# Kernel tuning notes

Measured on AMD Instinct MI355X. Metric: run time of the kernel, lower is better.

Reference implementation:

```python
import jax, jax.numpy as jnp
import numpy as np

# Problem sizes (see shape_source)
C = 4096                      # sparse matrix is C x C
NUMEL = C * C                 # 16,777,216
S = 3355443                   # round(NUMEL * 0.2) sampled gradient entries
R = 1048576                   # result_quantity (top-k buffer size)
DECAY = 0.95                  # decay_constant
FRAC = S / float(NUMEL)       # fractional_sparsity (mask_active=False branch)


def setup_inputs() -> dict:
    key = jax.random.key(0)
    k1, k2, k3, k4 = jax.random.split(key, 4)
    # Sampled linear indices into the C x C grid (forward: torch.randint(0, numel, [S]))
    sample_index = jax.random.randint(k1, (S,), 0, NUMEL, dtype=jnp.int32)
    # Steady-state buffer of (row, col) pairs and their running gradient magnitudes
    result_index = jax.random.randint(k2, (R, 2), 0, C, dtype=jnp.int32)
    result_value = jax.random.uniform(k3, (R,), dtype=jnp.float32)
    # Incoming gradient on the sampled accumulator entries
    gradient = jax.random.normal(k4, (S,), dtype=jnp.float32)
    return {
        "sample_index": sample_index,
        "result_index": result_index,
        "result_value": result_value,
        "gradient": gradient,
    }


def reference(sample_index, result_index, result_value, gradient):
    """Faithful JAX version of StochasticSubSampler's backward-hook update:
    decay the stored buffer, take |gradient| on the new samples, coalesce
    duplicated (row, col) entries by summation, then keep the top-R values.
    Returns (new_result_index [R,2] int32, new_result_value [R] float32)."""
    adj_decay = 1.0 - FRAC * (1.0 - DECAY)  # adjusted decay constant

    # Linearized keys for coalescing. sample_index is already row*C + col.
    samp_keys = sample_index
    res_keys = result_index[:, 0] * C + result_index[:, 1]
    keys = jnp.concatenate([samp_keys, res_keys])               # [K]
    vals = jnp.concatenate([jnp.abs(gradient), adj_decay * result_value])  # [K]
    K = keys.shape[0]

    # Coalesce: sum values that share the same (row, col) key.
    uniq, inv = jnp.unique(keys, size=K, fill_value=-1, return_inverse=True)
    summed = jax.ops.segment_sum(vals, inv, num_segments=K)     # [K]
    counts = jax.ops.segment_sum(jnp.ones_like(vals), inv, num_segments=K)
    neg = jnp.finfo(jnp.float32).min
    summed = jnp.where(counts > 0, summed, neg)  # mask padded unique slots

    # Descending sort + top-R selection (argsort(-v)[:R] in the original).
    top_vals, top_pos = jax.lax.top_k(summed, R)
    top_keys = uniq[top_pos]
    new_index = jnp.stack([top_keys // C, top_keys % C], axis=-1)  # [R, 2]
    return new_index, top_vals
```

## Files before the change

kernel.cpp:

```cpp
#include <hip/hip_runtime.h>
#include <stdint.h>

#define CDIM   4096
#define S_N    3355443
#define R_N    1048576
#define N1     (S_N + R_N)
#define TILE   4096
#define NTILES ((N1 + TILE - 1) / TILE)
#define NPAD   (NTILES * TILE)
#define NSB    (NPAD / 256)
#define PAD_KEY 0xFFFFFFu
#define PAD_VAL 0xFFFFFFFFu

static __device__ __forceinline__ unsigned blockScanExcl(unsigned v, unsigned t,
                                                         unsigned* lw, unsigned* tot){
  unsigned lane = t & 63u, w = t >> 6;
  unsigned x = v;
  #pragma unroll
  for (int off = 1; off < 64; off <<= 1){
    unsigned y = __shfl_up(x, off, 64);
    if (lane >= (unsigned)off) x += y;
  }
  if (lane == 63u) lw[w] = x;
  __syncthreads();
  unsigned woff = 0;
  for (unsigned i = 0; i < w; i++) woff += lw[i];
  *tot = lw[0] + lw[1] + lw[2] + lw[3];
  __syncthreads();
  return x + woff - v;
}

__global__ __launch_bounds__(256) void k_build(const int* __restrict__ sidx,
                                               const int* __restrict__ ridx,
                                               const float* __restrict__ rval,
                                               const float* __restrict__ grad,
                                               uint64_t* __restrict__ A){
  unsigned i = blockIdx.x * 256u + threadIdx.x;
  uint32_t key, vb;
  if (i < S_N){
    key = (uint32_t)sidx[i];
    vb  = __float_as_uint(fabsf(grad[i]));
  } else if (i < N1){
    unsigned j = i - S_N;
    key = (uint32_t)(ridx[2u*j] * CDIM + ridx[2u*j + 1u]);
    const float ADJF = (float)(1.0 - (3355443.0 / 16777216.0) * (1.0 - 0.95));
    vb = __float_as_uint(ADJF * rval[j]);
  } else {
    key = PAD_KEY; vb = PAD_VAL;
  }
  A[i] = ((uint64_t)key << 32) | (uint64_t)vb;
}

__global__ __launch_bounds__(256) void k_hist(const uint64_t* __restrict__ in, unsigned shift,
                                              unsigned* __restrict__ gh){
  __shared__ unsigned h[256];
  unsigned t = threadIdx.x;
  h[t] = 0; __syncthreads();
  size_t base = (size_t)blockIdx.x * TILE;
  #pragma unroll
  for (int r = 0; r < 16; r++){
    uint64_t e = in[base + (size_t)r*256 + t];
    atomicAdd(&h[(unsigned)((e >> shift) & 0xFF)], 1u);
  }
  __syncthreads();
  gh[t * NTILES + blockIdx.x] = h[t];
}

__global__ __launch_bounds__(256) void k_scanrows(unsigned* __restrict__ gh,
                                                  unsigned* __restrict__ dtot){
  __shared__ unsigned lw[4];
  unsigned d = blockIdx.x, t = threadIdx.x;
  unsigned carry = 0;
  for (unsigned base = 0; base < NTILES; base += 256){
    unsigned i = base + t;
    unsigned v = (i < NTILES) ? gh[d * NTILES + i] : 0u;
    unsigned tot;
    unsigned e = blockScanExcl(v, t, lw, &tot);
    if (i < NTILES) gh[d * NTILES + i] = e + carry;
    carry += tot;
  }
  if (t == 0) dtot[d] = carry;
}

template <bool FINAL>
__device__ __forceinline__ void scatter_body(const uint64_t* __restrict__ in,
                                             uint64_t* __restrict__ out,
                                             float* __restrict__ fout,
                                             unsigned shift,
                                             const unsigned* __restrict__ gh,
                                             const unsigned* __restrict__ dtot){
  __shared__ unsigned wrun[4*256];
  __shared__ unsigned gput[256];
  __shared__ unsigned lw[4];
  __shared__ uint64_t stage[TILE];
  unsigned t = threadIdx.x, lane = t & 63u, w = t >> 6;
  wrun[t] = 0; wrun[256+t] = 0; wrun[512+t] = 0; wrun[768+t] = 0;
  __syncthreads();
  uint64_t ltm = (lane == 0) ? 0ull : (~0ull >> (64u - lane));
  uint64_t elems[16]; unsigned rnk[16]; unsigned dg[16];
  size_t base = (size_t)blockIdx.x * TILE + (size_t)w * 1024;
  #pragma unroll
  for (int r = 0; r < 16; r++){
    uint64_t e = in[base + (size_t)r*64 + lane];
    elems[r] = e;
    unsigned d = (unsigned)((e >> shift) & 0xFF);
    uint64_t m = ~0ull;
    #pragma unroll
    for (int b = 0; b < 8; b++){
      uint64_t bb = __ballot((d >> b) & 1u);
      m &= ((d >> b) & 1u) ? bb : ~bb;
    }
    unsigned rr   = (unsigned)__popcll(m & ltm);
    unsigned prev = wrun[w*256 + d];
    __builtin_amdgcn_wave_barrier();
    if (rr == 0) wrun[w*256 + d] = prev + (unsigned)__popcll(m);
    __builtin_amdgcn_wave_barrier();
    rnk[r] = prev + rr;
    dg[r]  = d;
  }
  __syncthreads();
  {
    unsigned d = t;
    unsigned c0 = wrun[d], c1 = wrun[256+d], c2 = wrun[512+d], c3 = wrun[768+d];
    unsigned cnt = c0 + c1 + c2 + c3;
    unsigned tot;
    unsigned ldig  = blockScanExcl(cnt, t, lw, &tot);
    unsigned tot2;
    unsigned dbase = blockScanExcl(dtot[d], t, lw, &tot2);
    gput[d] = dbase + gh[d * NTILES + blockIdx.x] - ldig;
    wrun[d]       = ldig;
    wrun[256 + d] = ldig + c0;
    wrun[512 + d] = ldig + c0 + c1;
    wrun[768 + d] = ldig + c0 + c1 + c2;
  }
  __syncthreads();
  #pragma unroll
  for (int r = 0; r < 16; r++)
    stage[ wrun[w*256 + dg[r]] + rnk[r] ] = elems[r];
  __syncthreads();
  #pragma unroll
  for (int r = 0; r < 16; r++){
    unsigned j = (unsigned)r * 256u + t;
    uint64_t e = stage[j];
    unsigned d = (unsigned)((e >> shift) & 0xFF);
    unsigned dest = gput[d] + j;
    if (FINAL){
      if (dest < R_N){
        uint32_t key = (uint32_t)(e >> 32);
        fout[2u*dest]        = (float)(key >> 12);
        fout[2u*dest + 1u]   = (float)(key & 4095u);
        fout[2u*R_N + dest]  = __uint_as_float(~(uint32_t)e);
      }
    } else {
      out[dest] = e;
    }
  }
}

__global__ __launch_bounds__(256) void k_scatter(const uint64_t* __restrict__ in,
                                                 uint64_t* __restrict__ out,
                                                 unsigned shift,
                                                 const unsigned* __restrict__ gh,
                                                 const unsigned* __restrict__ dtot){
  scatter_body<false>(in, out, nullptr, shift, gh, dtot);
}

__global__ __launch_bounds__(256) void k_scatter_out(const uint64_t* __restrict__ in,
                                                     float* __restrict__ fout,
                                                     unsigned shift,
                                                     const unsigned* __restrict__ gh,
                                                     const unsigned* __restrict__ dtot){
  scatter_body<true>(in, nullptr, fout, shift, gh, dtot);
}

__global__ __launch_bounds__(256) void k_headcount(const uint64_t* __restrict__ in,
                                                   unsigned* __restrict__ hcnt){
  __shared__ unsigned wc[4];
  unsigned t = threadIdx.x, lane = t & 63u, w = t >> 6;
  size_t p = (size_t)blockIdx.x * 256 + t;
  uint64_t e = in[p];
  uint32_t k = (uint32_t)(e >> 32);
  bool head = ((p == 0) || ((uint32_t)(in[p-1] >> 32) != k)) && ((uint32_t)e != PAD_VAL);
  uint64_t m = __ballot(head);
  if (lane == 0) wc[w] = (unsigned)__popcll(m);
  __syncthreads();
  if (t == 0) hcnt[blockIdx.x] = wc[0] + wc[1] + wc[2] + wc[3];
}

__global__ __launch_bounds__(256) void k_scanheads(unsigned* __restrict__ hcnt,
                                                   unsigned* __restrict__ utot){
  __shared__ unsigned short buf[NSB];
  __shared__ unsigned lw[4];
  unsigned t = threadIdx.x;
  for (unsigned i = t; i < NSB; i += 256) buf[i] = (unsigned short)hcnt[i];
  __syncthreads();
  const unsigned CH = (NSB + 255) / 256;
  unsigned s = 0;
  for (unsigned k = 0; k < CH; k++){
    unsigned i = t * CH + k;
    if (i < NSB) s += buf[i];
  }
  unsigned tot;
  unsigned carry = blockScanExcl(s, t, lw, &tot);
  for (unsigned k = 0; k < CH; k++){
    unsigned i = t * CH + k;
    if (i < NSB){ unsigned v = buf[i]; hcnt[i] = carry; carry += v; }
  }
  if (t == 0) utot[0] = tot;
}

__global__ __launch_bounds__(256) void k_fill_tail(uint64_t* __restrict__ A,
                                                   const unsigned* __restrict__ utot){
  unsigned U = utot[0];
  unsigned i = blockIdx.x * 256u + threadIdx.x;
  if (i >= U) A[i] = ((uint64_t)PAD_KEY << 32) | (uint64_t)PAD_VAL;
}

__global__ __launch_bounds__(256) void k_segsum(const uint64_t* __restrict__ in,
                                                uint64_t* __restrict__ out,
                                                const unsigned* __restrict__ hbase){
  __shared__ unsigned wc[4], woffs[4];
  unsigned t = threadIdx.x, lane = t & 63u, w = t >> 6;
  size_t p = (size_t)blockIdx.x * 256 + t;
  uint64_t e0 = in[p];
  uint32_t k = (uint32_t)(e0 >> 32);
  bool head = ((p == 0) || ((uint32_t)(in[p-1] >> 32) != k)) && ((uint32_t)e0 != PAD_VAL);
  uint64_t m = __ballot(head);
  if (lane == 0) wc[w] = (unsigned)__popcll(m);
  __syncthreads();
  if (t == 0){ unsigned a = 0; for (int i = 0; i < 4; i++){ woffs[i] = a; a += wc[i]; } }
  __syncthreads();
  if (head){
    uint64_t ltm = (lane == 0) ? 0ull : (~0ull >> (64u - lane));
    unsigned rank = (unsigned)__popcll(m & ltm);
    unsigned oidx = hbase[blockIdx.x] + woffs[w] + rank;
    float s = __uint_as_float((uint32_t)e0);
    size_t q = p + 1;
    while (q < NPAD){
      uint64_t e = in[q];
      if ((uint32_t)(e >> 32) != k) break;
      uint32_t vb = (uint32_t)e;
      if (vb == PAD_VAL) break;
      s += __uint_as_float(vb);
      q++;
    }
    out[oidx] = ((uint64_t)k << 32) | (uint64_t)(uint32_t)(~__float_as_uint(s));
  }
}

extern "C" void kernel_launch(void* const* d_in, const int* in_sizes, int n_in,
                              void* d_out, int out_size, void* d_ws, size_t ws_size,
                              hipStream_t stream) {
  const int*   sidx = (const int*)d_in[0];
  const int*   ridx = (const int*)d_in[1];
  const float* rval = (const float*)d_in[2];
  const float* grad = (const float*)d_in[3];
  float* out = (float*)d_out;

  uint64_t* A0   = (uint64_t*)d_ws;
  uint64_t* A1   = A0 + NPAD;
  unsigned* gh   = (unsigned*)(A1 + NPAD);
  unsigned* dtot = gh + 256 * NTILES;
  unsigned* hcnt = dtot + 256;
  unsigned* utot = hcnt + NSB;

  k_build<<<NSB, 256, 0, stream>>>(sidx, ridx, rval, grad, A0);

  k_hist    <<<NTILES, 256, 0, stream>>>(A0, 32, gh);
  k_scanrows<<<256,    256, 0, stream>>>(gh, dtot);
  k_scatter <<<NTILES, 256, 0, stream>>>(A0, A1, 32, gh, dtot);
  k_hist    <<<NTILES, 256, 0, stream>>>(A1, 40, gh);
  k_scanrows<<<256,    256, 0, stream>>>(gh, dtot);
  k_scatter <<<NTILES, 256, 0, stream>>>(A1, A0, 40, gh, dtot);
  k_hist    <<<NTILES, 256, 0, stream>>>(A0, 48, gh);
  k_scanrows<<<256,    256, 0, stream>>>(gh, dtot);
  k_scatter <<<NTILES, 256, 0, stream>>>(A0, A1, 48, gh, dtot);

  k_headcount<<<NSB, 256, 0, stream>>>(A1, hcnt);
  k_scanheads<<<1,   256, 0, stream>>>(hcnt, utot);
  k_fill_tail<<<NSB, 256, 0, stream>>>(A0, utot);
  k_segsum   <<<NSB, 256, 0, stream>>>(A1, A0, hcnt);

  k_hist    <<<NTILES, 256, 0, stream>>>(A0, 0, gh);
  k_scanrows<<<256,    256, 0, stream>>>(gh, dtot);
  k_scatter <<<NTILES, 256, 0, stream>>>(A0, A1, 0, gh, dtot);
  k_hist    <<<NTILES, 256, 0, stream>>>(A1, 8, gh);
  k_scanrows<<<256,    256, 0, stream>>>(gh, dtot);
  k_scatter <<<NTILES, 256, 0, stream>>>(A1, A0, 8, gh, dtot);
  k_hist    <<<NTILES, 256, 0, stream>>>(A0, 16, gh);
  k_scanrows<<<256,    256, 0, stream>>>(gh, dtot);
  k_scatter <<<NTILES, 256, 0, stream>>>(A0, A1, 16, gh, dtot);
  k_hist       <<<NTILES, 256, 0, stream>>>(A1, 24, gh);
  k_scanrows   <<<256,    256, 0, stream>>>(gh, dtot);
  k_scatter_out<<<NTILES, 256, 0, stream>>>(A1, out, 24, gh, dtot);
}
```

Baseline: 433.4 us.

## Prefilter top-R candidates by value histogram and fuse histogram with row scans

```diff
diff --git a/kernel.cpp b/kernel.cpp
--- a/kernel.cpp
+++ b/kernel.cpp
@@ -6,11 +6,13 @@
 #define R_N    1048576
 #define N1     (S_N + R_N)
 #define TILE   4096
-#define NTILES ((N1 + TILE - 1) / TILE)
+#define NTILES 1076
 #define NPAD   (NTILES * TILE)
-#define NSB    (NPAD / 256)
+#define NT2    320
+#define SPAD   (NT2 * TILE)
 #define PAD_KEY 0xFFFFFFu
 #define PAD_VAL 0xFFFFFFFFu
+#define PADREC  ((((uint64_t)PAD_KEY) << 32) | (uint64_t)PAD_VAL)
 
 static __device__ __forceinline__ unsigned blockScanExcl(unsigned v, unsigned t,
                                                          unsigned* lw, unsigned* tot){
@@ -30,30 +32,77 @@
   return x + woff - v;
 }
 
-__global__ __launch_bounds__(256) void k_build(const int* __restrict__ sidx,
-                                               const int* __restrict__ ridx,
-                                               const float* __restrict__ rval,
-                                               const float* __restrict__ grad,
-                                               uint64_t* __restrict__ A){
+static __device__ __forceinline__ void block_signal(unsigned* cnt, unsigned* ord_sh){
+  __syncthreads();
+  if (threadIdx.x == 0)
+    *ord_sh = __hip_atomic_fetch_add(cnt, 1u, __ATOMIC_ACQ_REL, __HIP_MEMORY_SCOPE_AGENT);
+  __syncthreads();
+}
+static __device__ __forceinline__ void spin_until(unsigned* cnt, unsigned total){
+  if (threadIdx.x == 0){
+    while (__hip_atomic_load(cnt, __ATOMIC_ACQUIRE, __HIP_MEMORY_SCOPE_AGENT) < total)
+      __builtin_amdgcn_s_sleep(1);
+  }
+  __syncthreads();
+}
+static __device__ __forceinline__ void scan_row(unsigned* gh, unsigned* dtot, unsigned nt){
+  __shared__ unsigned lw_sr[4];
+  unsigned d = blockIdx.x, t = threadIdx.x;
+  unsigned carry = 0;
+  for (unsigned base = 0; base < nt; base += 256){
+    unsigned i = base + t;
+    unsigned v = (i < nt) ? gh[d*nt + i] : 0u;
+    unsigned tot; unsigned e = blockScanExcl(v, t, lw_sr, &tot);
+    if (i < nt) gh[d*nt + i] = e + carry;
+    carry += tot;
+  }
+  if (t == 0) dtot[d] = carry;
+}
+
+__global__ __launch_bounds__(256) void k_zero(unsigned* __restrict__ p, unsigned n){
   unsigned i = blockIdx.x * 256u + threadIdx.x;
-  uint32_t key, vb;
-  if (i < S_N){
-    key = (uint32_t)sidx[i];
-    vb  = __float_as_uint(fabsf(grad[i]));
-  } else if (i < N1){
-    unsigned j = i - S_N;
-    key = (uint32_t)(ridx[2u*j] * CDIM + ridx[2u*j + 1u]);
-    const float ADJF = (float)(1.0 - (3355443.0 / 16777216.0) * (1.0 - 0.95));
-    vb = __float_as_uint(ADJF * rval[j]);
-  } else {
-    key = PAD_KEY; vb = PAD_VAL;
-  }
-  A[i] = ((uint64_t)key << 32) | (uint64_t)vb;
-}
-
-__global__ __launch_bounds__(256) void k_hist(const uint64_t* __restrict__ in, unsigned shift,
-                                              unsigned* __restrict__ gh){
+  if (i < n) p[i] = 0u;
+}
+
+__global__ __launch_bounds__(256, 6) void k_build_hs(const int* __restrict__ sidx,
+    const int* __restrict__ ridx, const float* __restrict__ rval,
+    const float* __restrict__ grad, uint64_t* __restrict__ A,
+    unsigned* __restrict__ gh, unsigned* __restrict__ dtot, unsigned* __restrict__ cnt){
   __shared__ unsigned h[256];
+  __shared__ unsigned ord;
+  unsigned t = threadIdx.x;
+  h[t] = 0; __syncthreads();
+  unsigned base = blockIdx.x * (unsigned)TILE;
+  #pragma unroll
+  for (int r = 0; r < 16; r++){
+    unsigned i = base + (unsigned)r*256u + t;
+    uint32_t key, vb;
+    if (i < S_N){
+      key = (uint32_t)sidx[i];
+      vb  = __float_as_uint(fabsf(grad[i]));
+    } else if (i < N1){
+      unsigned j = i - S_N;
+      key = (uint32_t)(ridx[2u*j] * CDIM + ridx[2u*j + 1u]);
+      const float ADJF = (float)(1.0 - (3355443.0 / 16777216.0) * (1.0 - 0.95));
+      vb = __float_as_uint(ADJF * rval[j]);
+    } else { key = PAD_KEY; vb = PAD_VAL; }
+    A[i] = ((uint64_t)key << 32) | (uint64_t)vb;
+    atomicAdd(&h[key & 0xFFu], 1u);
+  }
+  __syncthreads();
+  gh[t*NTILES + blockIdx.x] = h[t];
+  block_signal(cnt, &ord);
+  if (blockIdx.x < 256){
+    spin_until(cnt, NTILES);
+    scan_row(gh, dtot, NTILES);
+  }
+}
+
+__global__ __launch_bounds__(256, 6) void k_hist_s(const uint64_t* __restrict__ in,
+    unsigned shift, unsigned* __restrict__ gh, unsigned* __restrict__ dtot,
+    unsigned* __restrict__ cnt, unsigned nt){
+  __shared__ unsigned h[256];
+  __shared__ unsigned ord;
   unsigned t = threadIdx.x;
   h[t] = 0; __syncthreads();
   size_t base = (size_t)blockIdx.x * TILE;
@@ -63,23 +112,12 @@
     atomicAdd(&h[(unsigned)((e >> shift) & 0xFF)], 1u);
   }
   __syncthreads();
-  gh[t * NTILES + blockIdx.x] = h[t];
-}
-
-__global__ __launch_bounds__(256) void k_scanrows(unsigned* __restrict__ gh,
-                                                  unsigned* __restrict__ dtot){
-  __shared__ unsigned lw[4];
-  unsigned d = blockIdx.x, t = threadIdx.x;
-  unsigned carry = 0;
-  for (unsigned base = 0; base < NTILES; base += 256){
-    unsigned i = base + t;
-    unsigned v = (i < NTILES) ? gh[d * NTILES + i] : 0u;
-    unsigned tot;
-    unsigned e = blockScanExcl(v, t, lw, &tot);
-    if (i < NTILES) gh[d * NTILES + i] = e + carry;
-    carry += tot;
-  }
-  if (t == 0) dtot[d] = carry;
+  gh[t*nt + blockIdx.x] = h[t];
+  block_signal(cnt, &ord);
+  if (blockIdx.x < 256){
+    spin_until(cnt, nt);
+    scan_row(gh, dtot, nt);
+  }
 }
 
 template <bool FINAL>
@@ -88,7 +126,8 @@
                                              float* __restrict__ fout,
                                              unsigned shift,
                                              const unsigned* __restrict__ gh,
-                                             const unsigned* __restrict__ dtot){
+                                             const unsigned* __restrict__ dtot,
+                                             unsigned nt){
   __shared__ unsigned wrun[4*256];
   __shared__ unsigned gput[256];
   __shared__ unsigned lw[4];
@@ -122,12 +161,11 @@
   {
     unsigned d = t;
     unsigned c0 = wrun[d], c1 = wrun[256+d], c2 = wrun[512+d], c3 = wrun[768+d];
-    unsigned cnt = c0 + c1 + c2 + c3;
-    unsigned tot;
-    unsigned ldig  = blockScanExcl(cnt, t, lw, &tot);
-    unsigned tot2;
+    unsigned cnt_ = c0 + c1 + c2 + c3;
+    unsigned tot, tot2;
+    unsigned ldig  = blockScanExcl(cnt_, t, lw, &tot);
     unsigned dbase = blockScanExcl(dtot[d], t, lw, &tot2);
-    gput[d] = dbase + gh[d * NTILES + blockIdx.x] - ldig;
+    gput[d] = dbase + gh[d * nt + blockIdx.x] - ldig;
     wrun[d]       = ldig;
     wrun[256 + d] = ldig + c0;
     wrun[512 + d] = ldig + c0 + c1;
@@ -158,94 +196,167 @@
 }
 
 __global__ __launch_bounds__(256) void k_scatter(const uint64_t* __restrict__ in,
-                                                 uint64_t* __restrict__ out,
-                                                 unsigned shift,
-                                                 const unsigned* __restrict__ gh,
-                                                 const unsigned* __restrict__ dtot){
-  scatter_body<false>(in, out, nullptr, shift, gh, dtot);
-}
-
+    uint64_t* __restrict__ out, unsigned shift, const unsigned* __restrict__ gh,
+    const unsigned* __restrict__ dtot, unsigned nt){
+  scatter_body<false>(in, out, nullptr, shift, gh, dtot, nt);
+}
 __global__ __launch_bounds__(256) void k_scatter_out(const uint64_t* __restrict__ in,
-                                                     float* __restrict__ fout,
-                                                     unsigned shift,
-                                                     const unsigned* __restrict__ gh,
-                                                     const unsigned* __restrict__ dtot){
-  scatter_body<true>(in, nullptr, fout, shift, gh, dtot);
-}
-
-__global__ __launch_bounds__(256) void k_headcount(const uint64_t* __restrict__ in,
-                                                   unsigned* __restrict__ hcnt){
-  __shared__ unsigned wc[4];
+    float* __restrict__ fout, unsigned shift, const unsigned* __restrict__ gh,
+    const unsigned* __restrict__ dtot, unsigned nt){
+  scatter_body<true>(in, nullptr, fout, shift, gh, dtot, nt);
+}
+
+__global__ __launch_bounds__(256) void k_segsum12(const uint64_t* __restrict__ in,
+    uint64_t* __restrict__ out, unsigned short* __restrict__ g12){
+  __shared__ unsigned h12[4096];
+  unsigned t = threadIdx.x;
+  for (unsigned j = t; j < 4096u; j += 256u) h12[j] = 0;
+  __syncthreads();
+  size_t base = (size_t)blockIdx.x * TILE;
+  for (int r = 0; r < 16; r++){
+    size_t p = base + (size_t)r*256 + t;
+    uint64_t e0 = in[p];
+    uint32_t k = (uint32_t)(e0 >> 32);
+    uint32_t vb0 = (uint32_t)e0;
+    bool head = ((p == 0) || ((uint32_t)(in[p-1] >> 32) != k)) && (vb0 != PAD_VAL);
+    uint64_t rec = PADREC;
+    if (head){
+      float s = __uint_as_float(vb0);
+      size_t q = p + 1;
+      while (q < NPAD){
+        uint64_t e = in[q];
+        if ((uint32_t)(e >> 32) != k) break;
+        uint32_t vb = (uint32_t)e;
+        if (vb == PAD_VAL) break;
+        s += __uint_as_float(vb);
+        q++;
+      }
+      uint32_t sk = ~__float_as_uint(s);
+      rec = ((uint64_t)k << 32) | (uint64_t)sk;
+      atomicAdd(&h12[sk >> 20], 1u);
+    }
+    out[p] = rec;
+  }
+  __syncthreads();
+  unsigned short* row = g12 + (size_t)blockIdx.x * 4096;
+  for (unsigned j = t; j < 4096u; j += 256u) row[j] = (unsigned short)h12[j];
+}
+
+__global__ __launch_bounds__(256) void k_fold12p(const unsigned short* __restrict__ g12,
+    unsigned* __restrict__ partial, unsigned* __restrict__ sel, unsigned* __restrict__ cnt){
+  __shared__ unsigned acc[4096];
+  __shared__ unsigned ord;
+  __shared__ unsigned lw[4];
+  __shared__ unsigned fl[4];
+  __shared__ unsigned thr_sh;
   unsigned t = threadIdx.x, lane = t & 63u, w = t >> 6;
-  size_t p = (size_t)blockIdx.x * 256 + t;
-  uint64_t e = in[p];
-  uint32_t k = (uint32_t)(e >> 32);
-  bool head = ((p == 0) || ((uint32_t)(in[p-1] >> 32) != k)) && ((uint32_t)e != PAD_VAL);
-  uint64_t m = __ballot(head);
-  if (lane == 0) wc[w] = (unsigned)__popcll(m);
-  __syncthreads();
-  if (t == 0) hcnt[blockIdx.x] = wc[0] + wc[1] + wc[2] + wc[3];
-}
-
-__global__ __launch_bounds__(256) void k_scanheads(unsigned* __restrict__ hcnt,
-                                                   unsigned* __restrict__ utot){
-  __shared__ unsigned short buf[NSB];
+  for (unsigned j = t; j < 4096u; j += 256u) acc[j] = 0;
+  __syncthreads();
+  unsigned t0 = blockIdx.x * 68u, t1 = min(t0 + 68u, (unsigned)NTILES);
+  for (unsigned tile = t0; tile < t1; tile++){
+    const unsigned short* row = g12 + (size_t)tile * 4096;
+    for (unsigned j = t; j < 4096u; j += 256u) acc[j] += row[j];
+  }
+  __syncthreads();
+  for (unsigned j = t; j < 4096u; j += 256u) partial[blockIdx.x*4096u + j] = acc[j];
+  block_signal(cnt, &ord);
+  if (ord == 15u){
+    for (unsigned j = t; j < 4096u; j += 256u){
+      unsigned s = 0;
+      for (unsigned i = 0; i < 16u; i++) s += partial[i*4096u + j];
+      acc[j] = s;
+    }
+    if (t == 0) thr_sh = 0xFFFFFFFFu;
+    __syncthreads();
+    unsigned carry = 0;
+    for (unsigned c = 0; c < 16u; c++){
+      unsigned v = acc[c*256u + t];
+      unsigned tot; unsigned e = blockScanExcl(v, t, lw, &tot);
+      bool f = (carry + e + v >= (unsigned)R_N);
+      uint64_t m = __ballot(f);
+      if (lane == 0)
+        fl[w] = m ? (w*64u + (unsigned)__ffsll((unsigned long long)m) - 1u) : 0xFFFFFFFFu;
+      __syncthreads();
+      if (t == 0 && thr_sh == 0xFFFFFFFFu){
+        unsigned bb = min(min(fl[0], fl[1]), min(fl[2], fl[3]));
+        if (bb != 0xFFFFFFFFu) thr_sh = c*256u + bb;
+      }
+      __syncthreads();
+      carry += tot;
+    }
+    if (t == 0) sel[0] = (thr_sh == 0xFFFFFFFFu) ? 4095u : thr_sh;
+  }
+}
+
+__global__ __launch_bounds__(256) void k_tilecnt_s(const unsigned short* __restrict__ g12,
+    const unsigned* __restrict__ sel, unsigned* __restrict__ ccnt,
+    unsigned* __restrict__ mtot, unsigned* __restrict__ cnt){
   __shared__ unsigned lw[4];
+  __shared__ unsigned ord;
+  __shared__ unsigned thr_sh;
+  __shared__ unsigned buf[NTILES];
   unsigned t = threadIdx.x;
-  for (unsigned i = t; i < NSB; i += 256) buf[i] = (unsigned short)hcnt[i];
-  __syncthreads();
-  const unsigned CH = (NSB + 255) / 256;
+  if (t == 0) thr_sh = sel[0];
+  __syncthreads();
+  unsigned thr = thr_sh;
+  const unsigned short* row = g12 + (size_t)blockIdx.x * 4096;
   unsigned s = 0;
-  for (unsigned k = 0; k < CH; k++){
-    unsigned i = t * CH + k;
-    if (i < NSB) s += buf[i];
-  }
-  unsigned tot;
-  unsigned carry = blockScanExcl(s, t, lw, &tot);
-  for (unsigned k = 0; k < CH; k++){
-    unsigned i = t * CH + k;
-    if (i < NSB){ unsigned v = buf[i]; hcnt[i] = carry; carry += v; }
-  }
-  if (t == 0) utot[0] = tot;
-}
-
-__global__ __launch_bounds__(256) void k_fill_tail(uint64_t* __restrict__ A,
-                                                   const unsigned* __restrict__ utot){
-  unsigned U = utot[0];
-  unsigned i = blockIdx.x * 256u + threadIdx.x;
-  if (i >= U) A[i] = ((uint64_t)PAD_KEY << 32) | (uint64_t)PAD_VAL;
-}
-
-__global__ __launch_bounds__(256) void k_segsum(const uint64_t* __restrict__ in,
-                                                uint64_t* __restrict__ out,
-                                                const unsigned* __restrict__ hbase){
-  __shared__ unsigned wc[4], woffs[4];
+  for (unsigned j = t; j <= thr; j += 256u) s += row[j];
+  unsigned tot; blockScanExcl(s, t, lw, &tot);
+  if (t == 0) ccnt[blockIdx.x] = tot;
+  block_signal(cnt, &ord);
+  if (ord == NTILES - 1u){
+    for (unsigned i = t; i < NTILES; i += 256u) buf[i] = ccnt[i];
+    __syncthreads();
+    unsigned carry = 0;
+    for (unsigned base = 0; base < NTILES; base += 256u){
+      unsigned i = base + t;
+      unsigned v = (i < NTILES) ? buf[i] : 0u;
+      unsigned tt; unsigned e = blockScanExcl(v, t, lw, &tt);
+      if (i < NTILES) ccnt[i] = carry + e;
+      carry += tt;
+    }
+    if (t == 0) mtot[0] = carry;
+  }
+}
+
+__global__ __launch_bounds__(256) void k_compact(const uint64_t* __restrict__ A0,
+    uint64_t* __restrict__ A1, const unsigned* __restrict__ cbase,
+    const unsigned* __restrict__ mtot, const unsigned* __restrict__ sel){
+  __shared__ unsigned wsum[4];
+  __shared__ unsigned thr_sh;
   unsigned t = threadIdx.x, lane = t & 63u, w = t >> 6;
-  size_t p = (size_t)blockIdx.x * 256 + t;
-  uint64_t e0 = in[p];
-  uint32_t k = (uint32_t)(e0 >> 32);
-  bool head = ((p == 0) || ((uint32_t)(in[p-1] >> 32) != k)) && ((uint32_t)e0 != PAD_VAL);
-  uint64_t m = __ballot(head);
-  if (lane == 0) wc[w] = (unsigned)__popcll(m);
-  __syncthreads();
-  if (t == 0){ unsigned a = 0; for (int i = 0; i < 4; i++){ woffs[i] = a; a += wc[i]; } }
-  __syncthreads();
-  if (head){
-    uint64_t ltm = (lane == 0) ? 0ull : (~0ull >> (64u - lane));
-    unsigned rank = (unsigned)__popcll(m & ltm);
-    unsigned oidx = hbase[blockIdx.x] + woffs[w] + rank;
-    float s = __uint_as_float((uint32_t)e0);
-    size_t q = p + 1;
-    while (q < NPAD){
-      uint64_t e = in[q];
-      if ((uint32_t)(e >> 32) != k) break;
-      uint32_t vb = (uint32_t)e;
-      if (vb == PAD_VAL) break;
-      s += __uint_as_float(vb);
-      q++;
-    }
-    out[oidx] = ((uint64_t)k << 32) | (uint64_t)(uint32_t)(~__float_as_uint(s));
-  }
+  if (t == 0) thr_sh = sel[0];
+  __syncthreads();
+  unsigned thr = thr_sh;
+  uint64_t ltm = (lane == 0) ? 0ull : (~0ull >> (64u - lane));
+  uint64_t e[16]; unsigned rnk[16]; unsigned qb = 0;
+  size_t base = (size_t)blockIdx.x * TILE + (size_t)w * 1024;
+  unsigned wcount = 0;
+  #pragma unroll
+  for (int r = 0; r < 16; r++){
+    uint64_t x = A0[base + (size_t)r*64 + lane];
+    e[r] = x;
+    bool q = ((((uint32_t)x) >> 20) <= thr);
+    uint64_t m = __ballot(q);
+    rnk[r] = wcount + (unsigned)__popcll(m & ltm);
+    wcount += (unsigned)__popcll(m);
+    qb |= (q ? 1u : 0u) << r;
+  }
+  if (lane == 0) wsum[w] = wcount;
+  __syncthreads();
+  unsigned woff = 0;
+  for (unsigned i = 0; i < w; i++) woff += wsum[i];
+  unsigned b0 = cbase[blockIdx.x] + woff;
+  #pragma unroll
+  for (int r = 0; r < 16; r++)
+    if ((qb >> r) & 1u){
+      unsigned dest = b0 + rnk[r];
+      if (dest < (unsigned)SPAD) A1[dest] = e[r];
+    }
+  unsigned M = mtot[0];
+  for (size_t p = (size_t)M + blockIdx.x*256u + t; p < (size_t)SPAD; p += (size_t)NTILES*256u)
+    A1[p] = PADREC;
 }
 
 extern "C" void kernel_launch(void* const* d_in, const int* in_sizes, int n_in,
@@ -257,40 +368,37 @@
   const float* grad = (const float*)d_in[3];
   float* out = (float*)d_out;
 
-  uint64_t* A0   = (uint64_t*)d_ws;
-  uint64_t* A1   = A0 + NPAD;
-  unsigned* gh   = (unsigned*)(A1 + NPAD);
-  unsigned* dtot = gh + 256 * NTILES;
-  unsigned* hcnt = dtot + 256;
-  unsigned* utot = hcnt + NSB;
-
-  k_build<<<NSB, 256, 0, stream>>>(sidx, ridx, rval, grad, A0);
-
-  k_hist    <<<NTILES, 256, 0, stream>>>(A0, 32, gh);
-  k_scanrows<<<256,    256, 0, stream>>>(gh, dtot);
-  k_scatter <<<NTILES, 256, 0, stream>>>(A0, A1, 32, gh, dtot);
-  k_hist    <<<NTILES, 256, 0, stream>>>(A1, 40, gh);
-  k_scanrows<<<256,    256, 0, stream>>>(gh, dtot);
-  k_scatter <<<NTILES, 256, 0, stream>>>(A1, A0, 40, gh, dtot);
-  k_hist    <<<NTILES, 256, 0, stream>>>(A0, 48, gh);
-  k_scanrows<<<256,    256, 0, stream>>>(gh, dtot);
-  k_scatter <<<NTILES, 256, 0, stream>>>(A0, A1, 48, gh, dtot);
-
-  k_headcount<<<NSB, 256, 0, stream>>>(A1, hcnt);
-  k_scanheads<<<1,   256, 0, stream>>>(hcnt, utot);
-  k_fill_tail<<<NSB, 256, 0, stream>>>(A0, utot);
-  k_segsum   <<<NSB, 256, 0, stream>>>(A1, A0, hcnt);
-
-  k_hist    <<<NTILES, 256, 0, stream>>>(A0, 0, gh);
-  k_scanrows<<<256,    256, 0, stream>>>(gh, dtot);
-  k_scatter <<<NTILES, 256, 0, stream>>>(A0, A1, 0, gh, dtot);
-  k_hist    <<<NTILES, 256, 0, stream>>>(A1, 8, gh);
-  k_scanrows<<<256,    256, 0, stream>>>(gh, dtot);
-  k_scatter <<<NTILES, 256, 0, stream>>>(A1, A0, 8, gh, dtot);
-  k_hist    <<<NTILES, 256, 0, stream>>>(A0, 16, gh);
-  k_scanrows<<<256,    256, 0, stream>>>(gh, dtot);
-  k_scatter <<<NTILES, 256, 0, stream>>>(A0, A1, 16, gh, dtot);
-  k_hist       <<<NTILES, 256, 0, stream>>>(A1, 24, gh);
-  k_scanrows   <<<256,    256, 0, stream>>>(gh, dtot);
-  k_scatter_out<<<NTILES, 256, 0, stream>>>(A1, out, 24, gh, dtot);
-}
+  uint64_t* A0      = (uint64_t*)d_ws;
+  uint64_t* A1      = A0 + NPAD;
+  unsigned* gh      = (unsigned*)(A1 + NPAD);
+  unsigned* dtot    = gh + 256 * NTILES;
+  unsigned* partial = dtot + 256;
+  unsigned* ccnt    = partial + 16*4096;
+  unsigned* mtot    = ccnt + NTILES;
+  unsigned* sel     = mtot + 1;
+  unsigned* cnts    = sel + 4;
+  unsigned short* g12 = (unsigned short*)(cnts + 16);
+
+  k_zero<<<1, 256, 0, stream>>>(sel, 20);
+
+  k_build_hs<<<NTILES, 256, 0, stream>>>(sidx, ridx, rval, grad, A0, gh, dtot, cnts + 0);
+  k_scatter <<<NTILES, 256, 0, stream>>>(A0, A1, 32, gh, dtot, NTILES);
+  k_hist_s  <<<NTILES, 256, 0, stream>>>(A1, 40, gh, dtot, cnts + 1, NTILES);
+  k_scatter <<<NTILES, 256, 0, stream>>>(A1, A0, 40, gh, dtot, NTILES);
+  k_hist_s  <<<NTILES, 256, 0, stream>>>(A0, 48, gh, dtot, cnts + 2, NTILES);
+  k_scatter <<<NTILES, 256, 0, stream>>>(A0, A1, 48, gh, dtot, NTILES);
+
+  k_segsum12 <<<NTILES, 256, 0, stream>>>(A1, A0, g12);
+  k_fold12p  <<<16,     256, 0, stream>>>(g12, partial, sel, cnts + 3);
+  k_tilecnt_s<<<NTILES, 256, 0, stream>>>(g12, sel, ccnt, mtot, cnts + 4);
+  k_compact  <<<NTILES, 256, 0, stream>>>(A0, A1, ccnt, mtot, sel);
+
+  k_hist_s     <<<NT2, 256, 0, stream>>>(A1, 0, gh, dtot, cnts + 5, NT2);
+  k_scatter    <<<NT2, 256, 0, stream>>>(A1, A0, 0, gh, dtot, NT2);
+  k_hist_s     <<<NT2, 256, 0, stream>>>(A0, 8, gh, dtot, cnts + 6, NT2);
+  k_scatter    <<<NT2, 256, 0, stream>>>(A0, A1, 8, gh, dtot, NT2);
+  k_hist_s     <<<NT2, 256, 0, stream>>>(A1, 16, gh, dtot, cnts + 7, NT2);
+  k_scatter    <<<NT2, 256, 0, stream>>>(A1, A0, 16, gh, dtot, NT2);
+  k_hist_s     <<<NT2, 256, 0, stream>>>(A0, 24, gh, dtot, cnts + 8, NT2);
+  k_scatter_out<<<NT2, 256, 0, stream>>>(A0, out, 24, gh, dtot, NT2);
+}
```

New measurement: 814.5 us. +87.9%, slower.
